# Performance work log

Measured on AMD Instinct MI355X. Metric: run time of the kernel, lower is better.

The kernel has to match this reference:

```python
import jax, jax.numpy as jnp
import numpy as np

NUM_NODES = 100000
NUM_EDGES = 3200000
NUM_GRAPHS = 512
IN_DIM, OUT_DIM = 128, 16
DIMS = [IN_DIM, 32, 48, 64]


def glorot(key, shape):
    lim = float(np.sqrt(6.0 / (shape[0] + shape[1])))
    return jax.random.uniform(key, shape, jnp.float32, -lim, lim)


def setup_inputs() -> dict:
    key = jax.random.key(0)
    ks = jax.random.split(key, 12)
    x = jax.random.normal(ks[0], (NUM_NODES, IN_DIM), jnp.float32)
    edge_index = jax.random.randint(ks[1], (2, NUM_EDGES), 0, NUM_NODES, jnp.int64)
    batch = jnp.sort(jax.random.randint(ks[2], (NUM_NODES,), 0, NUM_GRAPHS, jnp.int64))
    params = {}
    for i in range(3):
        params[f"W{i+1}"] = glorot(ks[3 + i], (DIMS[i], DIMS[i + 1]))
        params[f"b{i+1}"] = jnp.zeros((DIMS[i + 1],), jnp.float32)
    params["fc1_w"] = glorot(ks[6], (64, 32))
    params["fc1_b"] = jnp.zeros((32,), jnp.float32)
    params["fc2_w"] = glorot(ks[7], (32, OUT_DIM))
    params["fc2_b"] = jnp.zeros((OUT_DIM,), jnp.float32)
    return {"x": x, "edge_index": edge_index, "batch": batch, **params}


def gcn_conv(x, W, b, src, dst, deg_inv_sqrt):
    # h = x @ W; aggregate with symmetric normalization + self loops (PyG GCNConv)
    h = x @ W  # [N, out]
    norm = deg_inv_sqrt[src] * deg_inv_sqrt[dst]  # [E]
    msg = h[src] * norm[:, None]  # [E, out]  (gather)
    agg = jnp.zeros_like(h).at[dst].add(msg)  # scatter-add to targets
    self_loop = h * (deg_inv_sqrt * deg_inv_sqrt)[:, None]
    return agg + self_loop + b


def reference(x, edge_index, batch, W1, b1, W2, b2, W3, b3, fc1_w, fc1_b, fc2_w, fc2_b):
    src, dst = edge_index[0], edge_index[1]
    n = x.shape[0]
    # degree with self loops: deg[i] = in-degree + 1
    deg = jnp.zeros((n,), jnp.float32).at[dst].add(1.0) + 1.0
    dis = jax.lax.rsqrt(deg)
    h = jax.nn.relu(gcn_conv(x, W1, b1, src, dst, dis))
    h = jax.nn.relu(gcn_conv(h, W2, b2, src, dst, dis))
    h = jax.nn.relu(gcn_conv(h, W3, b3, src, dst, dis))
    # global mean pool per graph
    sums = jax.ops.segment_sum(h, batch, num_segments=NUM_GRAPHS)
    cnts = jax.ops.segment_sum(jnp.ones((n,), jnp.float32), batch, num_segments=NUM_GRAPHS)
    pooled = sums / jnp.maximum(cnts, 1.0)[:, None]  # [G, 64]
    z = jax.nn.relu(pooled @ fc1_w + fc1_b)
    logits = z @ fc2_w + fc2_b
    return jax.nn.softmax(logits, axis=1)
```

## Files before the change

### kernel.cpp

```cpp
#include <hip/hip_runtime.h>
#include <hip/hip_fp16.h>

static constexpr int NN = 100000;
static constexpr int NE = 3200000;
static constexpr int NG = 512;
static constexpr int NCB = 196;
static constexpr int CHK = 8192;
static constexpr int NCH = (NE + CHK - 1) / CHK;
static constexpr int NCNT = NCB * NCH;
static constexpr int SCAN_BLK = 2048;
static constexpr int NSB = (NCNT + SCAN_BLK - 1) / SCAN_BLK;
static constexpr int CAPE = 24576;

typedef float f32x2 __attribute__((ext_vector_type(2)));

__device__ __forceinline__ void set2_fp8x4(unsigned v, f32x2* a) {
    a[0] = __builtin_amdgcn_cvt_pk_f32_fp8((int)v, false);
    a[1] = __builtin_amdgcn_cvt_pk_f32_fp8((int)v, true);
}
__device__ __forceinline__ void acc2_fp8x4(unsigned v, f32x2* a) {
    a[0] += __builtin_amdgcn_cvt_pk_f32_fp8((int)v, false);
    a[1] += __builtin_amdgcn_cvt_pk_f32_fp8((int)v, true);
}
__device__ __forceinline__ unsigned pack_fp8x4(float a, float b, float c, float d) {
    int p = __builtin_amdgcn_cvt_pk_fp8_f32(a, b, 0, false);
    p = __builtin_amdgcn_cvt_pk_fp8_f32(c, d, p, true);
    return (unsigned)p;
}
__device__ __forceinline__ unsigned pkh2(float a, float b) {
    __half2 h = __floats2half2_rn(a, b);
    return *(unsigned*)&h;
}

__global__ __launch_bounds__(256) void k_histC(const int4* __restrict__ dst4,
                                               int* __restrict__ cntC, int e4) {
    __shared__ int h[NCB];
    for (int i = threadIdx.x; i < NCB; i += 256) h[i] = 0;
    __syncthreads();
    const int s4 = blockIdx.x * (CHK / 4), e4end = min(s4 + CHK / 4, e4);
    for (int i = s4 + threadIdx.x; i < e4end; i += 256) {
        int4 d = dst4[i];
        atomicAdd(&h[d.x >> 9], 1);
        atomicAdd(&h[d.y >> 9], 1);
        atomicAdd(&h[d.z >> 9], 1);
        atomicAdd(&h[d.w >> 9], 1);
    }
    __syncthreads();
    for (int i = threadIdx.x; i < NCB; i += 256)
        cntC[(size_t)i * NCH + blockIdx.x] = h[i];
}

__global__ __launch_bounds__(256) void k_scanA(const int* __restrict__ in,
                                               int* __restrict__ out,
                                               int* __restrict__ bsum, int n) {
    __shared__ int s[256];
    const int tid = threadIdx.x;
    const int base = blockIdx.x * SCAN_BLK + tid * 8;
    int v[8], t = 0;
#pragma unroll
    for (int c = 0; c < 8; c++) {
        int idx = base + c;
        v[c] = (idx < n) ? in[idx] : 0;
        t += v[c];
    }
    s[tid] = t;
    __syncthreads();
    for (int off = 1; off < 256; off <<= 1) {
        int x = (tid >= off) ? s[tid - off] : 0;
        __syncthreads();
        s[tid] += x;
        __syncthreads();
    }
    if (tid == 255) bsum[blockIdx.x] = s[255];
    int run = s[tid] - t;
#pragma unroll
    for (int c = 0; c < 8; c++) {
        int idx = base + c;
        if (idx < n) out[idx] = run;
        run += v[c];
    }
}

__global__ __launch_bounds__(256) void k_scanB(int* __restrict__ bsum, int nb) {
    __shared__ int s[256];
    const int tid = threadIdx.x;
    int v = (tid < nb) ? bsum[tid] : 0;
    s[tid] = v;
    __syncthreads();
    for (int off = 1; off < 256; off <<= 1) {
        int x = (tid >= off) ? s[tid - off] : 0;
        __syncthreads();
        s[tid] += x;
        __syncthreads();
    }
    if (tid < nb) bsum[tid] = s[tid] - v;
}

__global__ __launch_bounds__(256) void k_scatC(const int4* __restrict__ src4,
                                               const int4* __restrict__ dst4,
                                               const int* __restrict__ sc,
                                               const int* __restrict__ bsum,
                                               unsigned* __restrict__ tmp, int e4) {
    __shared__ int cur[NCB];
    for (int i = threadIdx.x; i < NCB; i += 256) {
        size_t idx = (size_t)i * NCH + blockIdx.x;
        cur[i] = sc[idx] + bsum[idx >> 11];
    }
    __syncthreads();
    const int s4 = blockIdx.x * (CHK / 4), e4end = min(s4 + CHK / 4, e4);
    for (int i = s4 + threadIdx.x; i < e4end; i += 256) {
        int4 d = dst4[i];
        int4 sv = src4[i];
        int p0 = atomicAdd(&cur[d.x >> 9], 1);
        tmp[p0] = ((unsigned)(d.x & 511) << 17) | (unsigned)sv.x;
        int p1 = atomicAdd(&cur[d.y >> 9], 1);
        tmp[p1] = ((unsigned)(d.y & 511) << 17) | (unsigned)sv.y;
        int p2 = atomicAdd(&cur[d.z >> 9], 1);
        tmp[p2] = ((unsigned)(d.z & 511) << 17) | (unsigned)sv.z;
        int p3 = atomicAdd(&cur[d.w >> 9], 1);
        tmp[p3] = ((unsigned)(d.w & 511) << 17) | (unsigned)sv.w;
    }
}

__global__ __launch_bounds__(1024) void k_fill512(const unsigned* __restrict__ tmp,
                                                  const int* __restrict__ sc,
                                                  const int* __restrict__ bsum,
                                                  int* __restrict__ csr,
                                                  int* __restrict__ degi,
                                                  int* __restrict__ offs,
                                                  float* __restrict__ dis,
                                                  int n, int etotal) {
    __shared__ unsigned eL[CAPE];
    __shared__ int cnt[512];
    __shared__ int s[512];
    __shared__ int cur[512];
    const int b = blockIdx.x, tid = threadIdx.x;
    if (tid < 512) cnt[tid] = 0;
    size_t i0 = (size_t)b * NCH;
    const int e0 = sc[i0] + bsum[i0 >> 11];
    int e1 = etotal;
    if (b + 1 < NCB) {
        size_t i1 = (size_t)(b + 1) * NCH;
        e1 = sc[i1] + bsum[i1 >> 11];
    }
    const int m = e1 - e0;
    const bool fits = (m <= CAPE);
    __syncthreads();
    if (fits) {
        for (int i = tid; i < m; i += 1024) {
            unsigned pk = tmp[e0 + i];
            eL[i] = pk;
            atomicAdd(&cnt[pk >> 17], 1);
        }
    } else {
        for (int e = e0 + tid; e < e1; e += 1024)
            atomicAdd(&cnt[tmp[e] >> 17], 1);
    }
    __syncthreads();
    int v = 0;
    if (tid < 512) { v = cnt[tid]; s[tid] = v; }
    __syncthreads();
    for (int off = 1; off < 512; off <<= 1) {
        int x = 0;
        if (tid < 512 && tid >= off) x = s[tid - off];
        __syncthreads();
        if (tid < 512) s[tid] += x;
        __syncthreads();
    }
    if (tid < 512) {
        int c = e0 + s[tid] - v;
        cur[tid] = c;
        int node = b * 512 + tid;
        if (node < n) {
            degi[node] = v;
            offs[node] = c;
            dis[node] = rsqrtf((float)v + 1.0f);
        }
    }
    __syncthreads();
    if (fits) {
        for (int i = tid; i < m; i += 1024) {
            unsigned pk = eL[i];
            int p = atomicAdd(&cur[pk >> 17], 1);
            csr[p] = (int)(pk & 0x1FFFFu);
        }
    } else {
        for (int e = e0 + tid; e < e1; e += 1024) {
            unsigned pk = tmp[e];
            int p = atomicAdd(&cur[pk >> 17], 1);
            csr[p] = (int)(pk & 0x1FFFFu);
        }
    }
}

__global__ __launch_bounds__(256) void k_gemm1(const float* __restrict__ X,
                                               const float* __restrict__ W,
                                               const float* __restrict__ dis,
                                               unsigned* __restrict__ H, int n) {
    constexpr int IN = 128, ROWS = 32;
    __shared__ float sW[IN * 32];
    __shared__ float sX[ROWS][IN];
    const int tid = threadIdx.x;
    for (int i = tid; i < IN * 32; i += 256) sW[i] = W[i];
    const int row0 = blockIdx.x * ROWS;
    const float4* X4 = (const float4*)X;
    for (int i = tid; i < ROWS * 32; i += 256) {
        int r = row0 + (i >> 5);
        float4 v = make_float4(0.f, 0.f, 0.f, 0.f);
        if (r < n) v = X4[(size_t)r * 32 + (i & 31)];
        ((float4*)&sX[i >> 5][0])[i & 31] = v;
    }
    __syncthreads();
    const int lr = tid >> 3;
    const int cg = tid & 7;
    const int gr = row0 + lr;
    float acc[4] = {0.f, 0.f, 0.f, 0.f};
#pragma unroll 8
    for (int k = 0; k < IN; k++) {
        float xv = sX[lr][k];
#pragma unroll
        for (int c = 0; c < 4; c++)
            acc[c] = fmaf(xv, sW[k * 32 + 4 * cg + c], acc[c]);
    }
    if (gr < n) {
        float dd = dis[gr];
        H[(size_t)gr * 8 + cg] =
            pack_fp8x4(acc[0] * dd, acc[1] * dd, acc[2] * dd, acc[3] * dd);
    }
}

__global__ __launch_bounds__(256) void k_pull2(
        const uint2* __restrict__ Hp, const int* __restrict__ offs,
        const int* __restrict__ degi, const int* __restrict__ csr,
        const float* __restrict__ dis, const float* __restrict__ b,
        uint2* __restrict__ A, int n) {
    const int group = threadIdx.x >> 2, j0 = threadIdx.x & 3;
    const int d = blockIdx.x * 64 + group;
    if (d >= n) return;
    f32x2 acc[4];
    uint2 sv = Hp[(size_t)d * 4 + j0];
    set2_fp8x4(sv.x, acc); set2_fp8x4(sv.y, acc + 2);
    int e = offs[d];
    const int end = e + degi[d];
    for (; e < end; e += 8) {
        uint2 v[8];
#pragma unroll
        for (int i = 0; i < 8; i++) {
            int ee = e + i;
            int idx = csr[min(ee, NE - 1)];
            uint2 t = Hp[(size_t)idx * 4 + j0];
            if (ee >= end) { t.x = 0u; t.y = 0u; }
            v[i] = t;
        }
#pragma unroll
        for (int i = 0; i < 8; i++) {
            acc2_fp8x4(v[i].x, acc); acc2_fp8x4(v[i].y, acc + 2);
        }
    }
    const float dd = dis[d];
    float r[8];
#pragma unroll
    for (int c = 0; c < 4; c++) {
        r[2 * c]     = fmaxf(fmaf(acc[c].x, dd, b[8 * j0 + 2 * c]), 0.f) * dd;
        r[2 * c + 1] = fmaxf(fmaf(acc[c].y, dd, b[8 * j0 + 2 * c + 1]), 0.f) * dd;
    }
    A[(size_t)d * 4 + j0] = make_uint2(pack_fp8x4(r[0], r[1], r[2], r[3]),
                                       pack_fp8x4(r[4], r[5], r[6], r[7]));
}

__global__ __launch_bounds__(256) void k_pullmm32(
        const uint2* __restrict__ Hp, const int* __restrict__ offs,
        const int* __restrict__ degi, const int* __restrict__ csr,
        const float* __restrict__ dis, const float* __restrict__ W,
        const float* __restrict__ b, unsigned* __restrict__ A, int n) {
    __shared__ float sW[32 * 48];
    __shared__ float rows[64][33];
    for (int i = threadIdx.x; i < 32 * 48; i += 256) sW[i] = W[i];
    const int group = threadIdx.x >> 2, j0 = threadIdx.x & 3;
    const int d = blockIdx.x * 64 + group;
    if (d < n) {
        f32x2 acc[4];
        uint2 sv = Hp[(size_t)d * 4 + j0];
        set2_fp8x4(sv.x, acc); set2_fp8x4(sv.y, acc + 2);
        int e = offs[d];
        const int end = e + degi[d];
        for (; e < end; e += 8) {
            uint2 v[8];
#pragma unroll
            for (int i = 0; i < 8; i++) {
                int ee = e + i;
                int idx = csr[min(ee, NE - 1)];
                uint2 t = Hp[(size_t)idx * 4 + j0];
                if (ee >= end) { t.x = 0u; t.y = 0u; }
                v[i] = t;
            }
#pragma unroll
            for (int i = 0; i < 8; i++) {
                acc2_fp8x4(v[i].x, acc); acc2_fp8x4(v[i].y, acc + 2);
            }
        }
        const float dd = dis[d];
#pragma unroll
        for (int c = 0; c < 4; c++) {
            rows[group][8 * j0 + 2 * c]     = acc[c].x * dd;
            rows[group][8 * j0 + 2 * c + 1] = acc[c].y * dd;
        }
    }
    __syncthreads();
    const int row0 = blockIdx.x * 64;
    const int nl = threadIdx.x & 63, cgb = threadIdx.x >> 6;
    const int gr = row0 + nl;
    if (gr < n) {
        const float4* sW4 = (const float4*)sW;
        float s[3][4];
#pragma unroll
        for (int o = 0; o < 3; o++)
#pragma unroll
            for (int c = 0; c < 4; c++) s[o][c] = b[12 * cgb + 4 * o + c];
#pragma unroll 8
        for (int k = 0; k < 32; k++) {
            float rv = rows[nl][k];
#pragma unroll
            for (int o = 0; o < 3; o++) {
                float4 w = sW4[k * 12 + cgb * 3 + o];
                s[o][0] = fmaf(rv, w.x, s[o][0]);
                s[o][1] = fmaf(rv, w.y, s[o][1]);
                s[o][2] = fmaf(rv, w.z, s[o][2]);
                s[o][3] = fmaf(rv, w.w, s[o][3]);
            }
        }
        const float dd2 = dis[gr];
#pragma unroll
        for (int o = 0; o < 3; o++) {
            float r0 = fmaxf(s[o][0], 0.f) * dd2;
            float r1 = fmaxf(s[o][1], 0.f) * dd2;
            float r2 = fmaxf(s[o][2], 0.f) * dd2;
            float r3 = fmaxf(s[o][3], 0.f) * dd2;
            A[(size_t)gr * 12 + cgb * 3 + o] = pack_fp8x4(r0, r1, r2, r3);
        }
    }
}

__global__ __launch_bounds__(256) void k_pullmm48(
        const uint4* __restrict__ Hp,
        const int* __restrict__ offs,
        const int* __restrict__ degi, const int* __restrict__ csr,
        const float* __restrict__ dis, const float* __restrict__ W,
        const float* __restrict__ b, __half* __restrict__ A, int n) {
    __shared__ float sW[48 * 64];
    __shared__ float rows[64][49];
    for (int i = threadIdx.x; i < 48 * 64; i += 256) sW[i] = W[i];
    const int group = threadIdx.x >> 2, j0 = threadIdx.x & 3;
    const int d = blockIdx.x * 64 + group;
    if (d < n && j0 < 3) {
        f32x2 acc[8];
        uint4 sv = Hp[(size_t)d * 3 + j0];
        set2_fp8x4(sv.x, acc);     set2_fp8x4(sv.y, acc + 2);
        set2_fp8x4(sv.z, acc + 4); set2_fp8x4(sv.w, acc + 6);
        int e = offs[d];
        const int end = e + degi[d];
        for (; e < end; e += 8) {
            uint4 v[8];
#pragma unroll
            for (int i = 0; i < 8; i++) {
                int ee = e + i;
                int idx = csr[min(ee, NE - 1)];
                uint4 t = Hp[(size_t)idx * 3 + j0];
                if (ee >= end) { t.x = 0u; t.y = 0u; t.z = 0u; t.w = 0u; }
                v[i] = t;
            }
#pragma unroll
            for (int i = 0; i < 8; i++) {
                acc2_fp8x4(v[i].x, acc);     acc2_fp8x4(v[i].y, acc + 2);
                acc2_fp8x4(v[i].z, acc + 4); acc2_fp8x4(v[i].w, acc + 6);
            }
        }
        const float dd = dis[d];
#pragma unroll
        for (int c = 0; c < 8; c++) {
            rows[group][16 * j0 + 2 * c]     = acc[c].x * dd;
            rows[group][16 * j0 + 2 * c + 1] = acc[c].y * dd;
        }
    }
    __syncthreads();
    const int row0 = blockIdx.x * 64;
    const int nl = threadIdx.x & 63, cgb = threadIdx.x >> 6;
    const int gr = row0 + nl;
    if (gr < n) {
        const float4* sW4 = (const float4*)sW;
        float s[4][4];
#pragma unroll
        for (int o = 0; o < 4; o++)
#pragma unroll
            for (int c = 0; c < 4; c++) s[o][c] = b[16 * cgb + 4 * o + c];
#pragma unroll 8
        for (int k = 0; k < 48; k++) {
            float rv = rows[nl][k];
#pragma unroll
            for (int o = 0; o < 4; o++) {
                float4 w = sW4[k * 16 + cgb * 4 + o];
                s[o][0] = fmaf(rv, w.x, s[o][0]);
                s[o][1] = fmaf(rv, w.y, s[o][1]);
                s[o][2] = fmaf(rv, w.z, s[o][2]);
                s[o][3] = fmaf(rv, w.w, s[o][3]);
            }
        }
        uint4 q0, q1;
        q0.x = pkh2(s[0][0], s[0][1]); q0.y = pkh2(s[0][2], s[0][3]);
        q0.z = pkh2(s[1][0], s[1][1]); q0.w = pkh2(s[1][2], s[1][3]);
        q1.x = pkh2(s[2][0], s[2][1]); q1.y = pkh2(s[2][2], s[2][3]);
        q1.z = pkh2(s[3][0], s[3][1]); q1.w = pkh2(s[3][2], s[3][3]);
        ((uint4*)A)[(size_t)gr * 8 + cgb * 2]     = q0;
        ((uint4*)A)[(size_t)gr * 8 + cgb * 2 + 1] = q1;
    }
}

__global__ __launch_bounds__(256) void k_poolhead(
        const __half* __restrict__ A3, const int* __restrict__ batch,
        const float* __restrict__ f1w, const float* __restrict__ f1b,
        const float* __restrict__ f2w, const float* __restrict__ f2b,
        float* __restrict__ out, int n, int ngr) {
    const int g = blockIdx.x;
    __shared__ int sb[2];
    if (threadIdx.x < 2) {
        int target = g + threadIdx.x;
        int lo = 0, hi = n;
        while (lo < hi) {
            int mid = (lo + hi) >> 1;
            if (batch[mid] < target) lo = mid + 1; else hi = mid;
        }
        sb[threadIdx.x] = lo;
    }
    __syncthreads();
    const int s = sb[0], e = sb[1];
    const int cg8 = threadIdx.x & 7;
    const int rr  = threadIdx.x >> 3;
    float sum[8] = {0.f, 0.f, 0.f, 0.f, 0.f, 0.f, 0.f, 0.f};
    for (int node = s + rr; node < e; node += 32) {
        uint4 v = *(const uint4*)(A3 + (size_t)node * 64 + cg8 * 8);
        unsigned w[4] = {v.x, v.y, v.z, v.w};
#pragma unroll
        for (int h = 0; h < 4; h++) {
            __half2 h2 = *(__half2*)&w[h];
            float2 f = __half22float2(h2);
            sum[2 * h]     += fmaxf(f.x, 0.f);
            sum[2 * h + 1] += fmaxf(f.y, 0.f);
        }
    }
    __shared__ float red[32][64];
#pragma unroll
    for (int h = 0; h < 8; h++) red[rr][cg8 * 8 + h] = sum[h];
    __syncthreads();
    __shared__ float p[64], z[32], lg[16];
    const int t = threadIdx.x;
    if (t < 64) {
        float acc = 0.f;
#pragma unroll 8
        for (int r = 0; r < 32; r++) acc += red[r][t];
        p[t] = acc / fmaxf((float)(e - s), 1.f);
    }
    __syncthreads();
    if (t < 32) {
        float acc = f1b[t];
        for (int k = 0; k < 64; k++) acc = fmaf(p[k], f1w[k * 32 + t], acc);
        z[t] = fmaxf(acc, 0.f);
    }
    __syncthreads();
    if (t < 16) {
        float acc = f2b[t];
        for (int k = 0; k < 32; k++) acc = fmaf(z[k], f2w[k * 16 + t], acc);
        lg[t] = acc;
    }
    __syncthreads();
    if (t < 16) {
        float m = lg[0];
        for (int i = 1; i < 16; i++) m = fmaxf(m, lg[i]);
        float sden = 0.f;
        for (int i = 0; i < 16; i++) sden += expf(lg[i] - m);
        out[g * 16 + t] = expf(lg[t] - m) / sden;
    }
}

extern "C" void kernel_launch(void* const* d_in, const int* in_sizes, int n_in,
                              void* d_out, int out_size, void* d_ws, size_t ws_size,
                              hipStream_t stream) {
    (void)in_sizes; (void)n_in; (void)out_size; (void)ws_size;
    const float* x     = (const float*)d_in[0];
    const int*   ei    = (const int*)d_in[1];
    const int*   batch = (const int*)d_in[2];
    const float* W1 = (const float*)d_in[3];
    const float* b1 = (const float*)d_in[4];
    const float* W2 = (const float*)d_in[5];  const float* b2 = (const float*)d_in[6];
    const float* W3 = (const float*)d_in[7];  const float* b3 = (const float*)d_in[8];
    const float* f1w = (const float*)d_in[9]; const float* f1b = (const float*)d_in[10];
    const float* f2w = (const float*)d_in[11];const float* f2b = (const float*)d_in[12];
    float* out = (float*)d_out;

    const int* src = ei;
    const int* dst = ei + NE;

    float* ws = (float*)d_ws;
    size_t o = 0;
    float* dis    = ws + o; o += NN;
    int*   degi   = (int*)(ws + o); o += NN;
    int*   offs   = (int*)(ws + o); o += NN;
    int*   cntC   = (int*)(ws + o); o += 76640;
    int*   sc     = (int*)(ws + o); o += 76640;
    int*   bsum   = (int*)(ws + o); o += 48;
    int*   csr    = (int*)(ws + o); o += NE;
    unsigned* TA  = (unsigned*)(ws + o); o += NE;
    unsigned* H1  = (unsigned*)(ws + o); o += NN * 8;
    unsigned* H2  = (unsigned*)(ws + o); o += NN * 8;
    unsigned* H3  = (unsigned*)(ws + o); o += NN * 12;

    unsigned* tmp = (unsigned*)TA;
    __half*   A3  = (__half*)TA;

    k_histC<<<NCH, 256, 0, stream>>>((const int4*)dst, cntC, NE / 4);
    k_scanA<<<NSB, 256, 0, stream>>>(cntC, sc, bsum, NCNT);
    k_scanB<<<1, 256, 0, stream>>>(bsum, NSB);
    k_scatC<<<NCH, 256, 0, stream>>>((const int4*)src, (const int4*)dst,
                                     sc, bsum, tmp, NE / 4);
    k_fill512<<<NCB, 1024, 0, stream>>>(tmp, sc, bsum, csr, degi, offs, dis, NN, NE);

    const int PGRID = (NN + 63) / 64;

    k_gemm1<<<(NN + 31) / 32, 256, 0, stream>>>(x, W1, dis, H1, NN);
    k_pull2<<<PGRID, 256, 0, stream>>>((const uint2*)H1, offs, degi, csr, dis, b1,
                                       (uint2*)H2, NN);

    k_pullmm32<<<PGRID, 256, 0, stream>>>((const uint2*)H2, offs, degi, csr, dis,
                                          W2, b2, H3, NN);

    k_pullmm48<<<PGRID, 256, 0, stream>>>(
        (const uint4*)H3, offs, degi, csr, dis, W3, b3, A3, NN);

    k_poolhead<<<NG, 256, 0, stream>>>(A3, batch, f1w, f1b, f2w, f2b, out, NN, NG);
}
```

Before: 327.4 us.

## Split layer-3 aggregation into feature-sliced pull kernel and separate matmul

The third-layer fp8 features are stored as three planar 16-feature slices instead of interleaved rows, and the fused pull+matmul kernel is split in two. A persistent-style pull kernel assigns each block to a single slice, so the gather working set per slice is smaller and more cache-friendly, with one thread per node instead of four-thread groups that left one lane idle. It writes fp16 intermediates to reused buffers, and a separate kernel does the 48x64 matmul. The cost is an extra kernel launch and an extra write and read of the fp16 intermediate.

Measured after the change: 383.8 us. +17.2%, slower.

```diff
diff --git a/kernel.cpp b/kernel.cpp
--- a/kernel.cpp
+++ b/kernel.cpp
@@ -11,6 +11,7 @@
 static constexpr int SCAN_BLK = 2048;
 static constexpr int NSB = (NCNT + SCAN_BLK - 1) / SCAN_BLK;
 static constexpr int CAPE = 24576;
+static constexpr int T3GRID = 1048;
 
 typedef float f32x2 __attribute__((ext_vector_type(2)));
 
@@ -336,25 +337,29 @@
             float r1 = fmaxf(s[o][1], 0.f) * dd2;
             float r2 = fmaxf(s[o][2], 0.f) * dd2;
             float r3 = fmaxf(s[o][3], 0.f) * dd2;
-            A[(size_t)gr * 12 + cgb * 3 + o] = pack_fp8x4(r0, r1, r2, r3);
-        }
-    }
-}
-
-__global__ __launch_bounds__(256) void k_pullmm48(
-        const uint4* __restrict__ Hp,
-        const int* __restrict__ offs,
-        const int* __restrict__ degi, const int* __restrict__ csr,
-        const float* __restrict__ dis, const float* __restrict__ W,
-        const float* __restrict__ b, __half* __restrict__ A, int n) {
-    __shared__ float sW[48 * 64];
-    __shared__ float rows[64][49];
-    for (int i = threadIdx.x; i < 48 * 64; i += 256) sW[i] = W[i];
-    const int group = threadIdx.x >> 2, j0 = threadIdx.x & 3;
-    const int d = blockIdx.x * 64 + group;
-    if (d < n && j0 < 3) {
+            int w = cgb * 3 + o;
+            A[(size_t)(w >> 2) * NN * 4 + (size_t)gr * 4 + (w & 3)] =
+                pack_fp8x4(r0, r1, r2, r3);
+        }
+    }
+}
+
+__global__ __launch_bounds__(256) void k_pull3(
+        const unsigned* __restrict__ H3,
+        const int* __restrict__ offs, const int* __restrict__ degi,
+        const int* __restrict__ csr, const float* __restrict__ dis,
+        unsigned* __restrict__ G0, unsigned* __restrict__ G1,
+        unsigned* __restrict__ G2, int n) {
+    const int s8 = blockIdx.x & 7;
+    const int slice = s8 % 3;
+    const int cnt = (slice < 2) ? 3 : 2;
+    const int rank = (blockIdx.x >> 3) * cnt + (s8 - slice) / 3;
+    const int stride = (int)(gridDim.x >> 3) * cnt * 256;
+    const uint4* P = (const uint4*)(H3 + (size_t)slice * NN * 4);
+    unsigned* G = (slice == 0) ? G0 : (slice == 1) ? G1 : G2;
+    for (int d = rank * 256 + threadIdx.x; d < n; d += stride) {
         f32x2 acc[8];
-        uint4 sv = Hp[(size_t)d * 3 + j0];
+        uint4 sv = P[d];
         set2_fp8x4(sv.x, acc);     set2_fp8x4(sv.y, acc + 2);
         set2_fp8x4(sv.z, acc + 4); set2_fp8x4(sv.w, acc + 6);
         int e = offs[d];
@@ -365,7 +370,7 @@
             for (int i = 0; i < 8; i++) {
                 int ee = e + i;
                 int idx = csr[min(ee, NE - 1)];
-                uint4 t = Hp[(size_t)idx * 3 + j0];
+                uint4 t = P[idx];
                 if (ee >= end) { t.x = 0u; t.y = 0u; t.z = 0u; t.w = 0u; }
                 v[i] = t;
             }
@@ -376,14 +381,38 @@
             }
         }
         const float dd = dis[d];
-#pragma unroll
-        for (int c = 0; c < 8; c++) {
-            rows[group][16 * j0 + 2 * c]     = acc[c].x * dd;
-            rows[group][16 * j0 + 2 * c + 1] = acc[c].y * dd;
-        }
-    }
-    __syncthreads();
+        unsigned g[8];
+#pragma unroll
+        for (int j = 0; j < 8; j++)
+            g[j] = pkh2(acc[j].x * dd, acc[j].y * dd);
+        uint4* Gq = (uint4*)(G + (size_t)d * 8);
+        Gq[0] = make_uint4(g[0], g[1], g[2], g[3]);
+        Gq[1] = make_uint4(g[4], g[5], g[6], g[7]);
+    }
+}
+
+__global__ __launch_bounds__(256) void k_mm48(
+        const unsigned* __restrict__ G0, const unsigned* __restrict__ G1,
+        const unsigned* __restrict__ G2, const float* __restrict__ W,
+        const float* __restrict__ b, __half* __restrict__ A, int n) {
+    __shared__ float sW[48 * 64];
+    __shared__ float rows[64][49];
+    for (int i = threadIdx.x; i < 48 * 64; i += 256) sW[i] = W[i];
     const int row0 = blockIdx.x * 64;
+    for (int i = threadIdx.x; i < 64 * 24; i += 256) {
+        int nl = i / 24, w = i % 24;
+        int pl = w >> 3, j = w & 7;
+        int node = row0 + nl;
+        if (node < n) {
+            const unsigned* gp = (pl == 0) ? G0 : (pl == 1) ? G1 : G2;
+            unsigned u = gp[(size_t)node * 8 + j];
+            __half2 h2 = *(__half2*)&u;
+            float2 f = __half22float2(h2);
+            rows[nl][pl * 16 + 2 * j]     = f.x;
+            rows[nl][pl * 16 + 2 * j + 1] = f.y;
+        }
+    }
+    __syncthreads();
     const int nl = threadIdx.x & 63, cgb = threadIdx.x >> 6;
     const int gr = row0 + nl;
     if (gr < n) {
@@ -512,9 +541,12 @@
     unsigned* H1  = (unsigned*)(ws + o); o += NN * 8;
     unsigned* H2  = (unsigned*)(ws + o); o += NN * 8;
     unsigned* H3  = (unsigned*)(ws + o); o += NN * 12;
+    unsigned* G2  = (unsigned*)(ws + o); o += NN * 8;
 
     unsigned* tmp = (unsigned*)TA;
     __half*   A3  = (__half*)TA;
+    unsigned* G0  = H1;
+    unsigned* G1  = H2;
 
     k_histC<<<NCH, 256, 0, stream>>>((const int4*)dst, cntC, NE / 4);
     k_scanA<<<NSB, 256, 0, stream>>>(cntC, sc, bsum, NCNT);
@@ -532,8 +564,8 @@
     k_pullmm32<<<PGRID, 256, 0, stream>>>((const uint2*)H2, offs, degi, csr, dis,
                                           W2, b2, H3, NN);
 
-    k_pullmm48<<<PGRID, 256, 0, stream>>>(
-        (const uint4*)H3, offs, degi, csr, dis, W3, b3, A3, NN);
+    k_pull3<<<T3GRID, 256, 0, stream>>>(H3, offs, degi, csr, dis, G0, G1, G2, NN);
+    k_mm48<<<PGRID, 256, 0, stream>>>(G0, G1, G2, W3, b3, A3, NN);
 
     k_poolhead<<<NG, 256, 0, stream>>>(A3, batch, f1w, f1b, f2w, f2b, out, NN, NG);
 }
```
